# Kernel optimization log

Hardware: AMD Instinct MI355X
Metric: run time of the kernel (lower is better)

The kernel has to match this reference:

```python
import jax, jax.numpy as jnp
import numpy as np

KSIZE = 7      # gaussian kernel size (SecondMomentMatrixLayer default)
SIGMA = 5.0    # gaussian sigma (default)
ALPHA = 0.05   # corner response alpha (CornerResponseLayer default)


def _gaussian_kernel(ksize, sigma):
    ax = np.arange(ksize, dtype=np.float64) - ksize // 2
    g1 = np.exp(-(ax ** 2) / (2.0 * sigma ** 2))
    k2 = np.outer(g1, g1)
    return (k2 / k2.sum()).astype(np.float32)


def setup_inputs() -> dict:
    key = jax.random.key(0)
    x = jax.random.normal(key, (4, 1, 2048, 2048), dtype=jnp.float32)
    # Sobel filters (ImageGradientsLayer): out-channels [Ix, Iy], shape (2,1,3,3)
    sobel_kernel = jnp.array(
        [[[[-1.0, 0.0, 1.0], [-2.0, 0.0, 2.0], [-1.0, 0.0, 1.0]]],
         [[[-1.0, -2.0, -1.0], [0.0, 0.0, 0.0], [1.0, 2.0, 1.0]]]],
        dtype=jnp.float32)
    # Depthwise (groups=3) gaussian kernel, shape (3,1,7,7)
    g = jnp.asarray(_gaussian_kernel(KSIZE, SIGMA))
    gauss_kernel = jnp.tile(g[None, None], (3, 1, 1, 1))
    return {"x": x, "sobel_kernel": sobel_kernel, "gauss_kernel": gauss_kernel}


def _conv(x, k, pad, groups=1):
    # torch Conv2d is cross-correlation; so is lax.conv_general_dilated
    return jax.lax.conv_general_dilated(
        x, k, window_strides=(1, 1), padding=[(pad, pad), (pad, pad)],
        dimension_numbers=("NCHW", "OIHW", "NCHW"), feature_group_count=groups)


def reference(x, sobel_kernel, gauss_kernel):
    # 1) image gradients via Sobel: (N,1,H,W) -> (N,2,H,W)
    grads = _conv(x, sobel_kernel, pad=1)
    Ix, Iy = grads[:, 0], grads[:, 1]
    # 2) channel products: I_xx, I_yy, I_xy -> (N,3,H,W)
    prods = jnp.stack([Ix * Ix, Iy * Iy, Ix * Iy], axis=1)
    # 3) gaussian-weighted second moments (depthwise conv, groups=3)
    S = _conv(prods, gauss_kernel, pad=KSIZE // 2, groups=3)
    Sxx, Syy, Sxy = S[:, 0], S[:, 1], S[:, 2]
    # 4) corner response R = det - alpha * trace^2 -> (N,1,H,W)
    trace = Sxx + Syy
    R = (Sxx * Syy - Sxy * Sxy - ALPHA * trace * trace)[:, None]
    # 5) NMS: global-median threshold, 7x7 stride-1 maxpool, binarize, scale by R
    median = jnp.quantile(R, 0.5, method="lower")  # torch.median = lower median
    thr = jnp.where(R < median, jnp.float32(0.0), R)
    pooled = jax.lax.reduce_window(
        thr, -jnp.inf, jax.lax.max, window_dimensions=(1, 1, 7, 7),
        window_strides=(1, 1, 1, 1),
        padding=[(0, 0), (0, 0), (3, 3), (3, 3)])
    binarized = jnp.where(thr == pooled, jnp.float32(1.0), jnp.float32(0.0))
    return binarized * R
```

## Files before the change

### kernel.cpp

```cpp
#include <hip/hip_runtime.h>
#include <math.h>

constexpr int IMH = 2048, IMW = 2048, NB = 4;
constexpr int NPIX = NB * IMH * IMW;
constexpr unsigned KSEL = 8388607u;

__device__ __forceinline__ unsigned f2u(float f) {
    unsigned b = __float_as_uint(f);
    return (b & 0x80000000u) ? ~b : (b | 0x80000000u);
}

__device__ __forceinline__ void gauss7(float* a) {
    const double g0 = 0.8352702114112720;
    const double g1 = 0.9231163463866358;
    const double g2 = 0.9801986733067553;
    const double s = 2.0 * (g0 + g1 + g2) + 1.0;
    const double inv = 1.0 / s;
    a[0] = a[6] = (float)(g0 * inv);
    a[1] = a[5] = (float)(g1 * inv);
    a[2] = a[4] = (float)(g2 * inv);
    a[3] = (float)inv;
}

__launch_bounds__(256, 3)
__global__ void harris_R(const float* __restrict__ x, float* __restrict__ Rout,
                         unsigned* __restrict__ hist) {
    __shared__ float smem[12616];
    float* SX   = smem;
    float* STH  = smem;
    float* SIXY = smem + 7296;
    unsigned* LH = (unsigned*)(smem + 7296);

    const int tid = threadIdx.x;
    const int x0 = blockIdx.x * 64, y0 = blockIdx.y * 32, b = blockIdx.z;
    const float* xb = x + (size_t)b * IMH * IMW;

    for (int i = tid; i < 40 * 72; i += 256) {
        int r = i / 72, c = i - r * 72;
        int gy = y0 - 4 + r, gx = x0 - 4 + c;
        float v = 0.0f;
        if ((unsigned)gy < (unsigned)IMH && (unsigned)gx < (unsigned)IMW) v = xb[(size_t)gy * IMW + gx];
        SX[i] = v;
    }
    __syncthreads();

    for (int i = tid; i < 38 * 70; i += 256) {
        int r = i / 70, c = i - r * 70;
        int gy = y0 - 3 + r, gx = x0 - 3 + c;
        float ix = 0.0f, iy = 0.0f;
        if ((unsigned)gy < (unsigned)IMH && (unsigned)gx < (unsigned)IMW) {
            const float* p = SX + r * 72 + c;
            float x00 = p[0],   x01 = p[1],   x02 = p[2];
            float x10 = p[72],                 x12 = p[74];
            float x20 = p[144], x21 = p[145], x22 = p[146];
            ix = (x02 + 2.0f * x12 + x22) - (x00 + 2.0f * x10 + x20);
            iy = (x20 + 2.0f * x21 + x22) - (x00 + 2.0f * x01 + x02);
        }
        SIXY[r * 140 + c * 2]     = ix;
        SIXY[r * 140 + c * 2 + 1] = iy;
    }
    __syncthreads();

    float a[7]; gauss7(a);

    for (int i = tid; i < 38 * 64; i += 256) {
        int r = i >> 6, c = i & 63;
        const float* p = SIXY + r * 140 + c * 2;
        float sxx = 0.f, syy = 0.f, sxy = 0.f;
        #pragma unroll
        for (int d = 0; d < 7; ++d) {
            float ix = p[2 * d], iy = p[2 * d + 1];
            float t = a[d] * ix;
            sxx += t * ix;
            sxy += t * iy;
            syy += (a[d] * iy) * iy;
        }
        float* q = STH + r * 192 + c * 3;
        q[0] = sxx; q[1] = syy; q[2] = sxy;
    }
    __syncthreads();

    for (int i = tid; i < 4096; i += 256) LH[i] = 0u;

    const int lx = tid & 63, rb = tid >> 6;
    float* Rb = Rout + (size_t)b * IMH * IMW;
    float rv[8];
    #pragma unroll
    for (int k = 0; k < 8; ++k) {
        int ro = rb + 4 * k;
        float sxx = 0.f, syy = 0.f, sxy = 0.f;
        #pragma unroll
        for (int d = 0; d < 7; ++d) {
            const float* q = STH + (ro + d) * 192 + lx * 3;
            sxx += a[d] * q[0];
            syy += a[d] * q[1];
            sxy += a[d] * q[2];
        }
        float tr = sxx + syy;
        float R = sxx * syy - sxy * sxy - 0.05f * tr * tr;
        rv[k] = R;
        Rb[(size_t)(y0 + ro) * IMW + (x0 + lx)] = R;
    }
    __syncthreads();

    #pragma unroll
    for (int k = 0; k < 8; ++k) atomicAdd(&LH[f2u(rv[k]) >> 20], 1u);
    __syncthreads();

    for (int i = tid; i < 4096; i += 256) { unsigned c = LH[i]; if (c) atomicAdd(&hist[i], c); }
}

__global__ void zero_kernel(unsigned* __restrict__ p, int n, int kidx, unsigned kval) {
    int i = blockIdx.x * blockDim.x + threadIdx.x;
    if (i < n) p[i] = (i == kidx) ? kval : 0u;
}

__global__ void hist2_kernel(const float* __restrict__ R, unsigned* __restrict__ hist,
                             const unsigned* __restrict__ sel) {
    __shared__ unsigned lh[4096];
    for (int i = threadIdx.x; i < 4096; i += 256) lh[i] = 0u;
    __syncthreads();
    const unsigned pref = sel[1];
    const float4* R4 = (const float4*)R;
    const int n4 = NPIX / 4;
    for (int i = blockIdx.x * 256 + threadIdx.x; i < n4; i += gridDim.x * 256) {
        float4 v = R4[i];
        unsigned u;
        u = f2u(v.x); if ((u >> 20) == pref) atomicAdd(&lh[(u >> 8) & 0xFFFu], 1u);
        u = f2u(v.y); if ((u >> 20) == pref) atomicAdd(&lh[(u >> 8) & 0xFFFu], 1u);
        u = f2u(v.z); if ((u >> 20) == pref) atomicAdd(&lh[(u >> 8) & 0xFFFu], 1u);
        u = f2u(v.w); if ((u >> 20) == pref) atomicAdd(&lh[(u >> 8) & 0xFFFu], 1u);
    }
    __syncthreads();
    for (int i = threadIdx.x; i < 4096; i += 256) { unsigned c = lh[i]; if (c) atomicAdd(&hist[i], c); }
}

__global__ void hist3_kernel(const float* __restrict__ R, unsigned* __restrict__ hist,
                             const unsigned* __restrict__ sel) {
    __shared__ unsigned lh[256];
    if (threadIdx.x < 256) lh[threadIdx.x] = 0u;
    __syncthreads();
    const unsigned pref = sel[1];
    const float4* R4 = (const float4*)R;
    const int n4 = NPIX / 4;
    for (int i = blockIdx.x * 256 + threadIdx.x; i < n4; i += gridDim.x * 256) {
        float4 v = R4[i];
        unsigned u;
        u = f2u(v.x); if ((u >> 8) == pref) atomicAdd(&lh[u & 0xFFu], 1u);
        u = f2u(v.y); if ((u >> 8) == pref) atomicAdd(&lh[u & 0xFFu], 1u);
        u = f2u(v.z); if ((u >> 8) == pref) atomicAdd(&lh[u & 0xFFu], 1u);
        u = f2u(v.w); if ((u >> 8) == pref) atomicAdd(&lh[u & 0xFFu], 1u);
    }
    __syncthreads();
    { unsigned c = lh[threadIdx.x]; if (c) atomicAdd(&hist[threadIdx.x], c); }
}

__global__ void select_kernel(const unsigned* __restrict__ hist, unsigned* __restrict__ sel,
                              int bpt, int bits, int final_stage) {
    __shared__ unsigned part[256];
    __shared__ unsigned grp[16];
    __shared__ int chs;
    __shared__ unsigned runs;
    const int t = threadIdx.x;
    const unsigned krem = sel[0];
    unsigned s = 0;
    for (int i = 0; i < bpt; ++i) s += hist[t * bpt + i];
    part[t] = s;
    __syncthreads();
    #pragma unroll
    for (int off = 1; off < 256; off <<= 1) {
        unsigned add = (t >= off) ? part[t - off] : 0u;
        __syncthreads();
        part[t] += add;
        __syncthreads();
    }
    unsigned incl = part[t];
    unsigned excl = incl - s;
    if (excl <= krem && krem < incl) { chs = t; runs = excl; }
    __syncthreads();
    int ch = chs;
    if (t < bpt) grp[t] = hist[ch * bpt + t];
    __syncthreads();
    if (t == 0) {
        unsigned r2 = runs; int bsel = ch * bpt;
        for (int j = 0; j < bpt; ++j) {
            unsigned h = grp[j];
            if (r2 + h > krem) { bsel = ch * bpt + j; break; }
            r2 += h;
        }
        sel[0] = krem - r2;
        unsigned pref = (sel[1] << bits) | (unsigned)bsel;
        sel[1] = pref;
        if (final_stage) {
            unsigned fb = (pref & 0x80000000u) ? (pref ^ 0x80000000u) : ~pref;
            ((float*)sel)[2] = __uint_as_float(fb);
        }
    }
}

__launch_bounds__(256, 7)
__global__ void harris_out(const float* __restrict__ R, const unsigned* __restrict__ sel,
                           float* __restrict__ out) {
    __shared__ float SR[38 * 72];
    __shared__ float SM[38 * 64];
    const float med = ((const float*)sel)[2];
    const int tid = threadIdx.x;
    const int x0 = blockIdx.x * 64, y0 = blockIdx.y * 32, b = blockIdx.z;
    const float* Rb = R + (size_t)b * IMH * IMW;

    for (int i = tid; i < 38 * 70; i += 256) {
        int r = i / 70, c = i - r * 70;
        int gy = y0 - 3 + r, gx = x0 - 3 + c;
        float v = -INFINITY;
        if ((unsigned)gy < (unsigned)IMH && (unsigned)gx < (unsigned)IMW) v = Rb[(size_t)gy * IMW + gx];
        SR[r * 72 + c] = v;
    }
    __syncthreads();

    for (int i = tid; i < 38 * 64; i += 256) {
        int r = i >> 6, c = i & 63;
        const float* p = SR + r * 72 + c;
        float m = -INFINITY;
        #pragma unroll
        for (int d = 0; d < 7; ++d) {
            float v = p[d];
            float t = (v < med) ? ((v == -INFINITY) ? -INFINITY : 0.0f) : v;
            m = fmaxf(m, t);
        }
        SM[i] = m;
    }
    __syncthreads();

    const int lx = tid & 63, rb = tid >> 6;
    float* ob = out + (size_t)b * IMH * IMW;
    #pragma unroll
    for (int k = 0; k < 8; ++k) {
        int r = rb + 4 * k;
        float pooled = -INFINITY;
        #pragma unroll
        for (int d = 0; d < 7; ++d) pooled = fmaxf(pooled, SM[(r + d) * 64 + lx]);
        float v = SR[(r + 3) * 72 + (lx + 3)];
        float t = (v < med) ? 0.0f : v;
        ob[(size_t)(y0 + r) * IMW + (x0 + lx)] = (t == pooled) ? v : 0.0f;
    }
}

extern "C" void kernel_launch(void* const* d_in, const int* in_sizes, int n_in,
                              void* d_out, int out_size, void* d_ws, size_t ws_size,
                              hipStream_t stream) {
    const float* x = (const float*)d_in[0];
    float* out = (float*)d_out;

    const size_t needed = (size_t)NPIX * 4 + (4096 + 4096 + 256 + 8) * 4;
    if (ws_size < needed) return;
    float* R = (float*)d_ws;
    unsigned* hbase = (unsigned*)((char*)d_ws + (size_t)NPIX * 4);
    unsigned* h1 = hbase;
    unsigned* h2 = hbase + 4096;
    unsigned* h3 = hbase + 8192;
    unsigned* sel = hbase + 8448;

    zero_kernel<<<(8456 + 255) / 256, 256, 0, stream>>>(hbase, 8456, 8448, KSEL);

    dim3 tgrid(IMW / 64, IMH / 32, NB);
    harris_R<<<tgrid, 256, 0, stream>>>(x, R, h1);

    select_kernel<<<1, 256, 0, stream>>>(h1, sel, 16, 12, 0);
    hist2_kernel<<<2048, 256, 0, stream>>>(R, h2, sel);
    select_kernel<<<1, 256, 0, stream>>>(h2, sel, 16, 12, 0);
    hist3_kernel<<<2048, 256, 0, stream>>>(R, h3, sel);
    select_kernel<<<1, 256, 0, stream>>>(h3, sel, 1, 8, 1);

    harris_out<<<tgrid, 256, 0, stream>>>(R, sel, out);
}
```

Baseline: 286.5 us.

## Shrink Harris tiles, add interior fast paths, register sliding windows, slotted histogram

The R-computation kernel now uses 64x16 tiles with less shared memory and a higher occupancy hint. It gets an interior-tile fast path for loading and Sobel, SoA shared layout for the second moments, and a register sliding window for the vertical gaussian. The global first-level histogram is spread over 8 slots per bin to reduce atomic contention, and the select kernel sums the slots. The NMS output kernel also gains an interior load path and a register-based log-step vertical max. Smaller tiles recompute more halo per output pixel, in exchange for higher occupancy and cheaper loads.

New measurement: 458.2 us. +59.9%, slower.

```diff
diff --git a/kernel.cpp b/kernel.cpp
--- a/kernel.cpp
+++ b/kernel.cpp
@@ -22,92 +22,142 @@
     a[3] = (float)inv;
 }
 
-__launch_bounds__(256, 3)
+__device__ __forceinline__ void sobel_at(const float* p, int stride, float& ix, float& iy) {
+    float x00 = p[0], x01 = p[1], x02 = p[2];
+    float x10 = p[stride], x12 = p[stride + 2];
+    float x20 = p[2 * stride], x21 = p[2 * stride + 1], x22 = p[2 * stride + 2];
+    ix = (x02 + 2.0f * x12 + x22) - (x00 + 2.0f * x10 + x20);
+    iy = (x20 + 2.0f * x21 + x22) - (x00 + 2.0f * x01 + x02);
+}
+
+__launch_bounds__(256, 5)
 __global__ void harris_R(const float* __restrict__ x, float* __restrict__ Rout,
                          unsigned* __restrict__ hist) {
-    __shared__ float smem[12616];
-    float* SX   = smem;
-    float* STH  = smem;
-    float* SIXY = smem + 7296;
-    unsigned* LH = (unsigned*)(smem + 7296);
+    __shared__ float smem[7392];
+    float* STH = smem;
+    float* SX = smem;
+    float* SIXY = smem + 4224;
+    unsigned* LH = (unsigned*)smem;
 
     const int tid = threadIdx.x;
-    const int x0 = blockIdx.x * 64, y0 = blockIdx.y * 32, b = blockIdx.z;
+    const int tx = tid & 63, ty = tid >> 6;
+    const int x0 = blockIdx.x * 64, y0 = blockIdx.y * 16, b = blockIdx.z;
     const float* xb = x + (size_t)b * IMH * IMW;
-
-    for (int i = tid; i < 40 * 72; i += 256) {
-        int r = i / 72, c = i - r * 72;
-        int gy = y0 - 4 + r, gx = x0 - 4 + c;
-        float v = 0.0f;
-        if ((unsigned)gy < (unsigned)IMH && (unsigned)gx < (unsigned)IMW) v = xb[(size_t)gy * IMW + gx];
-        SX[i] = v;
-    }
-    __syncthreads();
-
-    for (int i = tid; i < 38 * 70; i += 256) {
-        int r = i / 70, c = i - r * 70;
-        int gy = y0 - 3 + r, gx = x0 - 3 + c;
-        float ix = 0.0f, iy = 0.0f;
-        if ((unsigned)gy < (unsigned)IMH && (unsigned)gx < (unsigned)IMW) {
-            const float* p = SX + r * 72 + c;
-            float x00 = p[0],   x01 = p[1],   x02 = p[2];
-            float x10 = p[72],                 x12 = p[74];
-            float x20 = p[144], x21 = p[145], x22 = p[146];
-            ix = (x02 + 2.0f * x12 + x22) - (x00 + 2.0f * x10 + x20);
-            iy = (x20 + 2.0f * x21 + x22) - (x00 + 2.0f * x01 + x02);
-        }
-        SIXY[r * 140 + c * 2]     = ix;
-        SIXY[r * 140 + c * 2 + 1] = iy;
+    const bool interior = (x0 >= 4) && (x0 + 72 <= IMW) && (y0 >= 4) && (y0 + 20 <= IMH);
+
+    if (interior) {
+        const float* xb0 = xb + (size_t)(y0 - 4) * IMW + (x0 - 4);
+        #pragma unroll
+        for (int k = 0; k < 6; ++k) {
+            int r = ty + 4 * k;
+            SX[r * 76 + tx] = xb0[(size_t)r * IMW + tx];
+        }
+        for (int i = tid; i < 288; i += 256) {
+            int r = i / 12, c = 64 + (i - r * 12);
+            SX[r * 76 + c] = xb0[(size_t)r * IMW + c];
+        }
+    } else {
+        for (int i = tid; i < 24 * 76; i += 256) {
+            int r = i / 76, c = i - r * 76;
+            int gy = y0 - 4 + r, gx = x0 - 4 + c;
+            float v = 0.0f;
+            if ((unsigned)gy < (unsigned)IMH && (unsigned)gx < (unsigned)IMW)
+                v = xb[(size_t)gy * IMW + gx];
+            SX[r * 76 + c] = v;
+        }
+    }
+    __syncthreads();
+
+    float2* SI2 = (float2*)SIXY;
+    if (interior) {
+        #pragma unroll
+        for (int k = 0; k < 6; ++k) {
+            int r = ty + 4 * k;
+            if (r < 22) {
+                float ix, iy;
+                sobel_at(SX + r * 76 + tx, 76, ix, iy);
+                SI2[r * 72 + tx] = make_float2(ix, iy);
+            }
+        }
+        if (tid < 176) {
+            int r = tid >> 3, c = 64 + (tid & 7);
+            float ix, iy;
+            sobel_at(SX + r * 76 + c, 76, ix, iy);
+            SI2[r * 72 + c] = make_float2(ix, iy);
+        }
+    } else {
+        for (int i = tid; i < 22 * 72; i += 256) {
+            int r = i / 72, c = i - r * 72;
+            int gy = y0 - 3 + r, gx = x0 - 3 + c;
+            float ix = 0.0f, iy = 0.0f;
+            if ((unsigned)gy < (unsigned)IMH && (unsigned)gx < (unsigned)IMW)
+                sobel_at(SX + r * 76 + c, 76, ix, iy);
+            SI2[r * 72 + c] = make_float2(ix, iy);
+        }
     }
     __syncthreads();
 
     float a[7]; gauss7(a);
 
-    for (int i = tid; i < 38 * 64; i += 256) {
-        int r = i >> 6, c = i & 63;
-        const float* p = SIXY + r * 140 + c * 2;
+    #pragma unroll
+    for (int k = 0; k < 6; ++k) {
+        int r = ty + 4 * k;
+        if (r < 22) {
+            const float2* p = (const float2*)(SIXY + r * 144) + tx;
+            float sxx = 0.f, syy = 0.f, sxy = 0.f;
+            #pragma unroll
+            for (int d = 0; d < 7; ++d) {
+                float2 v = p[d];
+                float t = a[d] * v.x;
+                sxx += t * v.x;
+                sxy += t * v.y;
+                syy += (a[d] * v.y) * v.y;
+            }
+            STH[r * 64 + tx] = sxx;
+            STH[1408 + r * 64 + tx] = syy;
+            STH[2816 + r * 64 + tx] = sxy;
+        }
+    }
+    __syncthreads();
+
+    float vxx[10], vyy[10], vxy[10];
+    {
+        const float* base = STH + (4 * ty) * 64 + tx;
+        #pragma unroll
+        for (int t = 0; t < 10; ++t) {
+            vxx[t] = base[t * 64];
+            vyy[t] = base[1408 + t * 64];
+            vxy[t] = base[2816 + t * 64];
+        }
+    }
+    float rv[4];
+    float* Rb = Rout + (size_t)b * IMH * IMW + (size_t)y0 * IMW + x0;
+    #pragma unroll
+    for (int j = 0; j < 4; ++j) {
         float sxx = 0.f, syy = 0.f, sxy = 0.f;
         #pragma unroll
         for (int d = 0; d < 7; ++d) {
-            float ix = p[2 * d], iy = p[2 * d + 1];
-            float t = a[d] * ix;
-            sxx += t * ix;
-            sxy += t * iy;
-            syy += (a[d] * iy) * iy;
-        }
-        float* q = STH + r * 192 + c * 3;
-        q[0] = sxx; q[1] = syy; q[2] = sxy;
-    }
-    __syncthreads();
-
-    for (int i = tid; i < 4096; i += 256) LH[i] = 0u;
-
-    const int lx = tid & 63, rb = tid >> 6;
-    float* Rb = Rout + (size_t)b * IMH * IMW;
-    float rv[8];
-    #pragma unroll
-    for (int k = 0; k < 8; ++k) {
-        int ro = rb + 4 * k;
-        float sxx = 0.f, syy = 0.f, sxy = 0.f;
-        #pragma unroll
-        for (int d = 0; d < 7; ++d) {
-            const float* q = STH + (ro + d) * 192 + lx * 3;
-            sxx += a[d] * q[0];
-            syy += a[d] * q[1];
-            sxy += a[d] * q[2];
+            sxx += a[d] * vxx[j + d];
+            syy += a[d] * vyy[j + d];
+            sxy += a[d] * vxy[j + d];
         }
         float tr = sxx + syy;
         float R = sxx * syy - sxy * sxy - 0.05f * tr * tr;
-        rv[k] = R;
-        Rb[(size_t)(y0 + ro) * IMW + (x0 + lx)] = R;
-    }
-    __syncthreads();
-
-    #pragma unroll
-    for (int k = 0; k < 8; ++k) atomicAdd(&LH[f2u(rv[k]) >> 20], 1u);
-    __syncthreads();
-
-    for (int i = tid; i < 4096; i += 256) { unsigned c = LH[i]; if (c) atomicAdd(&hist[i], c); }
+        rv[j] = R;
+        Rb[(size_t)(4 * ty + j) * IMW + tx] = R;
+    }
+    __syncthreads();
+
+    for (int i = tid; i < 4096; i += 256) LH[i] = 0u;
+    __syncthreads();
+    #pragma unroll
+    for (int j = 0; j < 4; ++j) atomicAdd(&LH[f2u(rv[j]) >> 20], 1u);
+    __syncthreads();
+    const unsigned slot = ((blockIdx.z * gridDim.y + blockIdx.y) * gridDim.x + blockIdx.x) & 7u;
+    for (int i = tid; i < 4096; i += 256) {
+        unsigned c = LH[i];
+        if (c) atomicAdd(&hist[i * 8 + slot], c);
+    }
 }
 
 __global__ void zero_kernel(unsigned* __restrict__ p, int n, int kidx, unsigned kval) {
@@ -156,7 +206,7 @@
 }
 
 __global__ void select_kernel(const unsigned* __restrict__ hist, unsigned* __restrict__ sel,
-                              int bpt, int bits, int final_stage) {
+                              int bpt, int bits, int final_stage, int slots) {
     __shared__ unsigned part[256];
     __shared__ unsigned grp[16];
     __shared__ int chs;
@@ -164,7 +214,11 @@
     const int t = threadIdx.x;
     const unsigned krem = sel[0];
     unsigned s = 0;
-    for (int i = 0; i < bpt; ++i) s += hist[t * bpt + i];
+    for (int i = 0; i < bpt; ++i) {
+        unsigned bsum = 0;
+        for (int j = 0; j < slots; ++j) bsum += hist[(t * bpt + i) * slots + j];
+        s += bsum;
+    }
     part[t] = s;
     __syncthreads();
     #pragma unroll
@@ -179,7 +233,11 @@
     if (excl <= krem && krem < incl) { chs = t; runs = excl; }
     __syncthreads();
     int ch = chs;
-    if (t < bpt) grp[t] = hist[ch * bpt + t];
+    if (t < bpt) {
+        unsigned g = 0;
+        for (int j = 0; j < slots; ++j) g += hist[(ch * bpt + t) * slots + j];
+        grp[t] = g;
+    }
     __syncthreads();
     if (t == 0) {
         unsigned r2 = runs; int bsel = ch * bpt;
@@ -205,43 +263,66 @@
     __shared__ float SM[38 * 64];
     const float med = ((const float*)sel)[2];
     const int tid = threadIdx.x;
+    const int tx = tid & 63, ty = tid >> 6;
     const int x0 = blockIdx.x * 64, y0 = blockIdx.y * 32, b = blockIdx.z;
     const float* Rb = R + (size_t)b * IMH * IMW;
-
-    for (int i = tid; i < 38 * 70; i += 256) {
-        int r = i / 70, c = i - r * 70;
-        int gy = y0 - 3 + r, gx = x0 - 3 + c;
-        float v = -INFINITY;
-        if ((unsigned)gy < (unsigned)IMH && (unsigned)gx < (unsigned)IMW) v = Rb[(size_t)gy * IMW + gx];
-        SR[r * 72 + c] = v;
-    }
-    __syncthreads();
-
-    for (int i = tid; i < 38 * 64; i += 256) {
-        int r = i >> 6, c = i & 63;
-        const float* p = SR + r * 72 + c;
-        float m = -INFINITY;
-        #pragma unroll
-        for (int d = 0; d < 7; ++d) {
-            float v = p[d];
-            float t = (v < med) ? ((v == -INFINITY) ? -INFINITY : 0.0f) : v;
-            m = fmaxf(m, t);
-        }
-        SM[i] = m;
-    }
-    __syncthreads();
-
-    const int lx = tid & 63, rb = tid >> 6;
-    float* ob = out + (size_t)b * IMH * IMW;
-    #pragma unroll
-    for (int k = 0; k < 8; ++k) {
-        int r = rb + 4 * k;
-        float pooled = -INFINITY;
-        #pragma unroll
-        for (int d = 0; d < 7; ++d) pooled = fmaxf(pooled, SM[(r + d) * 64 + lx]);
-        float v = SR[(r + 3) * 72 + (lx + 3)];
+    const bool interior = (x0 >= 3) && (x0 + 67 <= IMW) && (y0 >= 3) && (y0 + 35 <= IMH);
+
+    if (interior) {
+        const float* Rb0 = Rb + (size_t)(y0 - 3) * IMW + (x0 - 3);
+        #pragma unroll
+        for (int k = 0; k < 10; ++k) {
+            int r = ty + 4 * k;
+            if (r < 38) SR[r * 72 + tx] = Rb0[(size_t)r * IMW + tx];
+        }
+        if (tid < 228) {
+            int r = tid / 6, c = 64 + (tid - r * 6);
+            SR[r * 72 + c] = Rb0[(size_t)r * IMW + c];
+        }
+    } else {
+        for (int i = tid; i < 38 * 70; i += 256) {
+            int r = i / 70, c = i - r * 70;
+            int gy = y0 - 3 + r, gx = x0 - 3 + c;
+            float v = -INFINITY;
+            if ((unsigned)gy < (unsigned)IMH && (unsigned)gx < (unsigned)IMW)
+                v = Rb[(size_t)gy * IMW + gx];
+            SR[r * 72 + c] = v;
+        }
+    }
+    __syncthreads();
+
+    #pragma unroll
+    for (int k = 0; k < 10; ++k) {
+        int r = ty + 4 * k;
+        if (r < 38) {
+            const float* p = SR + r * 72 + tx;
+            float m = -INFINITY;
+            #pragma unroll
+            for (int d = 0; d < 7; ++d) {
+                float v = p[d];
+                float t = (v < med) ? ((v == -INFINITY) ? -INFINITY : 0.0f) : v;
+                m = fmaxf(m, t);
+            }
+            SM[r * 64 + tx] = m;
+        }
+    }
+    __syncthreads();
+
+    float vm[14];
+    #pragma unroll
+    for (int t = 0; t < 14; ++t) vm[t] = SM[(8 * ty + t) * 64 + tx];
+    float m2[13], m4[11];
+    #pragma unroll
+    for (int i = 0; i < 13; ++i) m2[i] = fmaxf(vm[i], vm[i + 1]);
+    #pragma unroll
+    for (int i = 0; i < 11; ++i) m4[i] = fmaxf(m2[i], m2[i + 2]);
+    float* ob = out + (size_t)b * IMH * IMW + (size_t)y0 * IMW + x0;
+    #pragma unroll
+    for (int j = 0; j < 8; ++j) {
+        float pooled = fmaxf(m4[j], m4[j + 3]);
+        float v = SR[(8 * ty + j + 3) * 72 + (tx + 3)];
         float t = (v < med) ? 0.0f : v;
-        ob[(size_t)(y0 + r) * IMW + (x0 + lx)] = (t == pooled) ? v : 0.0f;
+        ob[(size_t)(8 * ty + j) * IMW + tx] = (t == pooled) ? v : 0.0f;
     }
 }
 
@@ -251,25 +332,26 @@
     const float* x = (const float*)d_in[0];
     float* out = (float*)d_out;
 
-    const size_t needed = (size_t)NPIX * 4 + (4096 + 4096 + 256 + 8) * 4;
+    const size_t needed = (size_t)NPIX * 4 + (32768 + 4096 + 256 + 8) * 4;
     if (ws_size < needed) return;
     float* R = (float*)d_ws;
     unsigned* hbase = (unsigned*)((char*)d_ws + (size_t)NPIX * 4);
     unsigned* h1 = hbase;
-    unsigned* h2 = hbase + 4096;
-    unsigned* h3 = hbase + 8192;
-    unsigned* sel = hbase + 8448;
-
-    zero_kernel<<<(8456 + 255) / 256, 256, 0, stream>>>(hbase, 8456, 8448, KSEL);
-
-    dim3 tgrid(IMW / 64, IMH / 32, NB);
-    harris_R<<<tgrid, 256, 0, stream>>>(x, R, h1);
-
-    select_kernel<<<1, 256, 0, stream>>>(h1, sel, 16, 12, 0);
+    unsigned* h2 = hbase + 32768;
+    unsigned* h3 = hbase + 36864;
+    unsigned* sel = hbase + 37120;
+
+    zero_kernel<<<(37128 + 255) / 256, 256, 0, stream>>>(hbase, 37128, 37120, KSEL);
+
+    dim3 rgrid(IMW / 64, IMH / 16, NB);
+    harris_R<<<rgrid, 256, 0, stream>>>(x, R, h1);
+
+    select_kernel<<<1, 256, 0, stream>>>(h1, sel, 16, 12, 0, 8);
     hist2_kernel<<<2048, 256, 0, stream>>>(R, h2, sel);
-    select_kernel<<<1, 256, 0, stream>>>(h2, sel, 16, 12, 0);
+    select_kernel<<<1, 256, 0, stream>>>(h2, sel, 16, 12, 0, 1);
     hist3_kernel<<<2048, 256, 0, stream>>>(R, h3, sel);
-    select_kernel<<<1, 256, 0, stream>>>(h3, sel, 1, 8, 1);
-
-    harris_out<<<tgrid, 256, 0, stream>>>(R, sel, out);
-}
+    select_kernel<<<1, 256, 0, stream>>>(h3, sel, 1, 8, 1, 1);
+
+    dim3 ogrid(IMW / 64, IMH / 32, NB);
+    harris_out<<<ogrid, 256, 0, stream>>>(R, sel, out);
+}
```
